# Kernel tuning notes

Hardware: AMD Instinct MI355X
Metric: run time of the kernel (lower is better)

## Reference

```python
import jax, jax.numpy as jnp
import numpy as np

WINDOW_SIZE = 11
SIGMA = 1.5
MAX_VAL = 1.0


def _gaussian_kernel2d(ws: int, sigma: float) -> jnp.ndarray:
    # matches kornia gaussian_t: x = arange(ws) - ws//2, normalized 1D, outer product
    x = jnp.arange(ws, dtype=jnp.float32) - ws // 2
    g = jnp.exp(-(x * x) / (2.0 * sigma * sigma))
    g = g / g.sum()
    return jnp.outer(g, g)  # (ws, ws)


def _filter2d(x: jnp.ndarray, kernel: jnp.ndarray) -> jnp.ndarray:
    # depthwise 'same' conv with reflect padding, matching kornia filter2d
    B, C, H, W = x.shape
    kh, kw = kernel.shape
    pad_h = ((kh - 1) // 2, (kh - 1) - (kh - 1) // 2)
    pad_w = ((kw - 1) // 2, (kw - 1) - (kw - 1) // 2)
    xp = jnp.pad(x, ((0, 0), (0, 0), pad_h, pad_w), mode='reflect')
    k = jnp.broadcast_to(kernel[None, None], (C, 1, kh, kw)).astype(x.dtype)
    return jax.lax.conv_general_dilated(
        xp, k, window_strides=(1, 1), padding='VALID',
        dimension_numbers=('NCHW', 'OIHW', 'NCHW'), feature_group_count=C)


def setup_inputs() -> dict:
    key = jax.random.key(0)
    k1, k2 = jax.random.split(key)
    img1 = jax.random.uniform(k1, (16, 3, 512, 512), dtype=jnp.float32)
    img2 = jax.random.uniform(k2, (16, 3, 512, 512), dtype=jnp.float32)
    kernel = _gaussian_kernel2d(WINDOW_SIZE, SIGMA)  # fixed gaussian window (11,11)
    return {"img1": img1, "img2": img2, "kernel": kernel}


def reference(img1, img2, kernel):
    C1 = (0.01 * MAX_VAL) ** 2
    C2 = (0.03 * MAX_VAL) ** 2
    mu1 = _filter2d(img1, kernel)
    mu2 = _filter2d(img2, kernel)
    mu1_sq = mu1 * mu1
    mu2_sq = mu2 * mu2
    mu1_mu2 = mu1 * mu2
    sigma1_sq = _filter2d(img1 * img1, kernel) - mu1_sq
    sigma2_sq = _filter2d(img2 * img2, kernel) - mu2_sq
    sigma12 = _filter2d(img1 * img2, kernel) - mu1_mu2
    num = (2.0 * mu1_mu2 + C1) * (2.0 * sigma12 + C2)
    den = (mu1_sq + mu2_sq + C1) * (sigma1_sq + sigma2_sq + C2)
    return num / den  # (B, C, H, W) SSIM map ('same' padding -> no crop)
```

## Files before the change

### kernel.cpp

```cpp
#include <hip/hip_runtime.h>

namespace {

constexpr int Hd = 512, Wd = 512;
constexpr int TH = 32;
constexpr int G  = 4;
constexpr int NG = TH / G;
constexpr int RAD = 5, WS = 11;
constexpr int NIN = G + WS - 1;
constexpr int HSTR = 524;
constexpr float C1c = 1e-4f;
constexpr float C2c = 9e-4f;

__device__ __forceinline__ float rcp_fast(float x) { return __builtin_amdgcn_rcpf(x); }

__global__ __launch_bounds__(512, 2) void ssim_map_kernel(
    const float* __restrict__ img1,
    const float* __restrict__ img2,
    const float* __restrict__ kern,
    float* __restrict__ out)
{
    __shared__ float hbuf[5 * G * HSTR];

    const int tid   = threadIdx.x;
    const int row0  = blockIdx.x * TH;
    const long pbase = (long)blockIdx.y * (long)(Hd * Wd);

    float g[WS];
    {
        float s = 0.f;
#pragma unroll
        for (int j = 0; j < WS; ++j) s += kern[RAD * WS + j];
        const float inv = 1.0f / s;
#pragma unroll
        for (int j = 0; j < WS; ++j) g[j] = kern[RAD * WS + j] * inv;
    }

    const int c  = tid;
    const int hr = tid >> 7;
    const int hu = tid & 127;

    for (int grp = 0; grp < NG; ++grp) {
        float acc[5][G];
#pragma unroll
        for (int q = 0; q < 5; ++q)
#pragma unroll
            for (int r = 0; r < G; ++r) acc[q][r] = 0.f;

        const int ibase = row0 + grp * G - RAD;
#pragma unroll
        for (int j = 0; j < NIN; ++j) {
            int gr = ibase + j;
            gr = (gr < 0) ? -gr : gr;
            gr = (gr >= Hd) ? (2 * Hd - 2 - gr) : gr;
            const long off = pbase + (long)gr * Wd + c;
            const float a = img1[off];
            const float b = img2[off];
            const float p11 = a * a, p22 = b * b, p12 = a * b;
#pragma unroll
            for (int r = 0; r < G; ++r) {
                const int k = j - r;
                if (k >= 0 && k < WS) {
                    const float w = g[k];
                    acc[0][r] = fmaf(w, a,   acc[0][r]);
                    acc[1][r] = fmaf(w, b,   acc[1][r]);
                    acc[2][r] = fmaf(w, p11, acc[2][r]);
                    acc[3][r] = fmaf(w, p22, acc[3][r]);
                    acc[4][r] = fmaf(w, p12, acc[4][r]);
                }
            }
        }

        __syncthreads();

#pragma unroll
        for (int q = 0; q < 5; ++q)
#pragma unroll
            for (int r = 0; r < G; ++r)
                hbuf[(q * G + r) * HSTR + RAD + c] = acc[q][r];

        if (c >= 1 && c <= RAD) {
#pragma unroll
            for (int q = 0; q < 5; ++q)
#pragma unroll
                for (int r = 0; r < G; ++r)
                    hbuf[(q * G + r) * HSTR + RAD - c] = acc[q][r];
        } else if (c >= Wd - 1 - RAD && c <= Wd - 2) {
#pragma unroll
            for (int q = 0; q < 5; ++q)
#pragma unroll
                for (int r = 0; r < G; ++r)
                    hbuf[(q * G + r) * HSTR + RAD + 1022 - c] = acc[q][r];
        }

        __syncthreads();

        float hq[5][4];
#pragma unroll
        for (int q = 0; q < 5; ++q) {
            const float* base = &hbuf[(q * G + hr) * HSTR + 4 * hu];
            const float4 v0 = *(const float4*)(base);
            const float4 v1 = *(const float4*)(base + 4);
            const float4 v2 = *(const float4*)(base + 8);
            const float2 v3 = *(const float2*)(base + 12);
            const float f[14] = { v0.x, v0.y, v0.z, v0.w,
                                  v1.x, v1.y, v1.z, v1.w,
                                  v2.x, v2.y, v2.z, v2.w,
                                  v3.x, v3.y };
            float h0 = 0.f, h1 = 0.f, h2 = 0.f, h3 = 0.f;
#pragma unroll
            for (int k = 0; k < WS; ++k) {
                const float w = g[k];
                h0 = fmaf(w, f[k],     h0);
                h1 = fmaf(w, f[k + 1], h1);
                h2 = fmaf(w, f[k + 2], h2);
                h3 = fmaf(w, f[k + 3], h3);
            }
            hq[q][0] = h0; hq[q][1] = h1; hq[q][2] = h2; hq[q][3] = h3;
        }

        float res[4];
#pragma unroll
        for (int j = 0; j < 4; ++j) {
            const float m1 = hq[0][j], m2 = hq[1][j];
            const float m1s = m1 * m1, m2s = m2 * m2, m12 = m1 * m2;
            const float sg1 = hq[2][j] - m1s;
            const float sg2 = hq[3][j] - m2s;
            const float sg12 = hq[4][j] - m12;
            const float num = (2.f * m12 + C1c) * (2.f * sg12 + C2c);
            const float den = (m1s + m2s + C1c) * (sg1 + sg2 + C2c);
            res[j] = num * rcp_fast(den);
        }
        float4* po = (float4*)&out[pbase + (long)(row0 + grp * G + hr) * Wd + 4 * hu];
        *po = make_float4(res[0], res[1], res[2], res[3]);
    }
}

}

extern "C" void kernel_launch(void* const* d_in, const int* in_sizes, int n_in,
                              void* d_out, int out_size, void* d_ws, size_t ws_size,
                              hipStream_t stream) {
    const float* img1 = (const float*)d_in[0];
    const float* img2 = (const float*)d_in[1];
    const float* kern = (const float*)d_in[2];
    float* outp = (float*)d_out;
    dim3 grid(Hd / TH, 48);
    ssim_map_kernel<<<grid, dim3(512), 0, stream>>>(img1, img2, kern, outp);
}
```

Measured before the change: 174.6 us.

## Tile SSIM kernel by column halves with packed f32x2 FMAs and split shared buffers

Splits each row band into two 256-column tiles, each run by a 256-thread block, so occupancy and block count rise. Each thread loads a halo column through reflect indexing instead of mirroring results into shared memory afterwards. The img1/img2 and squared channels are packed into float2 vectors so the compiler can emit packed FMA instructions. Shared memory is laid out as interleaved pairs to allow wider LDS reads. The cost is redundant vertical work on the 10 halo columns per tile and a second strided loop iteration for a few threads.

```diff
diff --git a/kernel.cpp b/kernel.cpp
--- a/kernel.cpp
+++ b/kernel.cpp
@@ -2,29 +2,38 @@
 
 namespace {
 
+typedef __attribute__((ext_vector_type(2))) float f32x2;
+typedef __attribute__((ext_vector_type(4))) float f32x4;
+
 constexpr int Hd = 512, Wd = 512;
+constexpr int TW = 256;
 constexpr int TH = 32;
 constexpr int G  = 4;
 constexpr int NG = TH / G;
 constexpr int RAD = 5, WS = 11;
 constexpr int NIN = G + WS - 1;
-constexpr int HSTR = 524;
+constexpr int SC  = TW + 2*RAD;
+constexpr int HSTR = 268;
 constexpr float C1c = 1e-4f;
 constexpr float C2c = 9e-4f;
 
 __device__ __forceinline__ float rcp_fast(float x) { return __builtin_amdgcn_rcpf(x); }
 
-__global__ __launch_bounds__(512, 2) void ssim_map_kernel(
+__global__ __launch_bounds__(256, 8) void ssim_map_kernel(
     const float* __restrict__ img1,
     const float* __restrict__ img2,
     const float* __restrict__ kern,
     float* __restrict__ out)
 {
-    __shared__ float hbuf[5 * G * HSTR];
+    __shared__ __align__(16) f32x2 hb01[G * HSTR];
+    __shared__ __align__(16) f32x2 hb23[G * HSTR];
+    __shared__ __align__(16) float hb4 [G * HSTR];
 
-    const int tid   = threadIdx.x;
-    const int row0  = blockIdx.x * TH;
-    const long pbase = (long)blockIdx.y * (long)(Hd * Wd);
+    const int tid  = threadIdx.x;
+    const int cb   = blockIdx.x;
+    const int row0 = blockIdx.y * TH;
+    const long pbase = (long)blockIdx.z * (long)(Hd * Wd);
+    const int col0 = cb * TW;
 
     float g[WS];
     {
@@ -36,103 +45,134 @@
         for (int j = 0; j < WS; ++j) g[j] = kern[RAD * WS + j] * inv;
     }
 
-    const int c  = tid;
-    const int hr = tid >> 7;
-    const int hu = tid & 127;
+    const int hr = tid >> 6;
+    const int hu = tid & 63;
 
     for (int grp = 0; grp < NG; ++grp) {
-        float acc[5][G];
-#pragma unroll
-        for (int q = 0; q < 5; ++q)
-#pragma unroll
-            for (int r = 0; r < G; ++r) acc[q][r] = 0.f;
+        __syncthreads();
 
         const int ibase = row0 + grp * G - RAD;
-#pragma unroll
-        for (int j = 0; j < NIN; ++j) {
-            int gr = ibase + j;
-            gr = (gr < 0) ? -gr : gr;
-            gr = (gr >= Hd) ? (2 * Hd - 2 - gr) : gr;
-            const long off = pbase + (long)gr * Wd + c;
-            const float a = img1[off];
-            const float b = img2[off];
-            const float p11 = a * a, p22 = b * b, p12 = a * b;
+        for (int s = tid; s < SC; s += 256) {
+            int gc = col0 - RAD + s;
+            gc = (gc < 0) ? -gc : gc;
+            gc = (gc >= Wd) ? (2 * Wd - 2 - gc) : gc;
+
+            f32x2 a01[G], a23[G]; float a4[G];
 #pragma unroll
             for (int r = 0; r < G; ++r) {
-                const int k = j - r;
-                if (k >= 0 && k < WS) {
-                    const float w = g[k];
-                    acc[0][r] = fmaf(w, a,   acc[0][r]);
-                    acc[1][r] = fmaf(w, b,   acc[1][r]);
-                    acc[2][r] = fmaf(w, p11, acc[2][r]);
-                    acc[3][r] = fmaf(w, p22, acc[3][r]);
-                    acc[4][r] = fmaf(w, p12, acc[4][r]);
+                a01[r].x = 0.f; a01[r].y = 0.f;
+                a23[r].x = 0.f; a23[r].y = 0.f;
+                a4[r] = 0.f;
+            }
+#pragma unroll
+            for (int j = 0; j < NIN; ++j) {
+                int gr = ibase + j;
+                gr = (gr < 0) ? -gr : gr;
+                gr = (gr >= Hd) ? (2 * Hd - 2 - gr) : gr;
+                const long off = pbase + (long)gr * Wd + gc;
+                const float a = img1[off];
+                const float b = img2[off];
+                f32x2 ab; ab.x = a; ab.y = b;
+                const f32x2 pp = ab * ab;
+                const float p12 = a * b;
+#pragma unroll
+                for (int r = 0; r < G; ++r) {
+                    const int k = j - r;
+                    if (k >= 0 && k < WS) {
+                        f32x2 w2; w2.x = g[k]; w2.y = g[k];
+                        a01[r] = __builtin_elementwise_fma(w2, ab, a01[r]);
+                        a23[r] = __builtin_elementwise_fma(w2, pp, a23[r]);
+                        a4[r]  = fmaf(g[k], p12, a4[r]);
+                    }
                 }
+            }
+#pragma unroll
+            for (int r = 0; r < G; ++r) {
+                hb01[r * HSTR + s] = a01[r];
+                hb23[r * HSTR + s] = a23[r];
+                hb4 [r * HSTR + s] = a4[r];
             }
         }
 
         __syncthreads();
 
+        f32x2 h01[4], h23[4];
+        float h4[4];
+        {
+            const f32x4* p4 = (const f32x4*)&hb01[hr * HSTR + 4 * hu];
+            f32x2 f[14];
 #pragma unroll
-        for (int q = 0; q < 5; ++q)
+            for (int i = 0; i < 7; ++i) {
+                const f32x4 t = p4[i];
+                f[2*i]   = t.lo;
+                f[2*i+1] = t.hi;
+            }
 #pragma unroll
-            for (int r = 0; r < G; ++r)
-                hbuf[(q * G + r) * HSTR + RAD + c] = acc[q][r];
-
-        if (c >= 1 && c <= RAD) {
+            for (int j = 0; j < 4; ++j) { h01[j].x = 0.f; h01[j].y = 0.f; }
 #pragma unroll
-            for (int q = 0; q < 5; ++q)
+            for (int k = 0; k < WS; ++k) {
+                f32x2 w2; w2.x = g[k]; w2.y = g[k];
 #pragma unroll
-                for (int r = 0; r < G; ++r)
-                    hbuf[(q * G + r) * HSTR + RAD - c] = acc[q][r];
-        } else if (c >= Wd - 1 - RAD && c <= Wd - 2) {
+                for (int j = 0; j < 4; ++j)
+                    h01[j] = __builtin_elementwise_fma(w2, f[k + j], h01[j]);
+            }
+        }
+        {
+            const f32x4* p4 = (const f32x4*)&hb23[hr * HSTR + 4 * hu];
+            f32x2 f[14];
 #pragma unroll
-            for (int q = 0; q < 5; ++q)
+            for (int i = 0; i < 7; ++i) {
+                const f32x4 t = p4[i];
+                f[2*i]   = t.lo;
+                f[2*i+1] = t.hi;
+            }
 #pragma unroll
-                for (int r = 0; r < G; ++r)
-                    hbuf[(q * G + r) * HSTR + RAD + 1022 - c] = acc[q][r];
+            for (int j = 0; j < 4; ++j) { h23[j].x = 0.f; h23[j].y = 0.f; }
+#pragma unroll
+            for (int k = 0; k < WS; ++k) {
+                f32x2 w2; w2.x = g[k]; w2.y = g[k];
+#pragma unroll
+                for (int j = 0; j < 4; ++j)
+                    h23[j] = __builtin_elementwise_fma(w2, f[k + j], h23[j]);
+            }
         }
-
-        __syncthreads();
-
-        float hq[5][4];
-#pragma unroll
-        for (int q = 0; q < 5; ++q) {
-            const float* base = &hbuf[(q * G + hr) * HSTR + 4 * hu];
-            const float4 v0 = *(const float4*)(base);
-            const float4 v1 = *(const float4*)(base + 4);
-            const float4 v2 = *(const float4*)(base + 8);
-            const float2 v3 = *(const float2*)(base + 12);
+        {
+            const float* base = &hb4[hr * HSTR + 4 * hu];
+            const f32x4 v0 = *(const f32x4*)(base);
+            const f32x4 v1 = *(const f32x4*)(base + 4);
+            const f32x4 v2 = *(const f32x4*)(base + 8);
+            const f32x2 v3 = *(const f32x2*)(base + 12);
             const float f[14] = { v0.x, v0.y, v0.z, v0.w,
                                   v1.x, v1.y, v1.z, v1.w,
                                   v2.x, v2.y, v2.z, v2.w,
                                   v3.x, v3.y };
-            float h0 = 0.f, h1 = 0.f, h2 = 0.f, h3 = 0.f;
+#pragma unroll
+            for (int j = 0; j < 4; ++j) h4[j] = 0.f;
 #pragma unroll
             for (int k = 0; k < WS; ++k) {
                 const float w = g[k];
-                h0 = fmaf(w, f[k],     h0);
-                h1 = fmaf(w, f[k + 1], h1);
-                h2 = fmaf(w, f[k + 2], h2);
-                h3 = fmaf(w, f[k + 3], h3);
+#pragma unroll
+                for (int j = 0; j < 4; ++j)
+                    h4[j] = fmaf(w, f[k + j], h4[j]);
             }
-            hq[q][0] = h0; hq[q][1] = h1; hq[q][2] = h2; hq[q][3] = h3;
         }
 
-        float res[4];
+        f32x4 res;
+        float rr[4];
 #pragma unroll
         for (int j = 0; j < 4; ++j) {
-            const float m1 = hq[0][j], m2 = hq[1][j];
-            const float m1s = m1 * m1, m2s = m2 * m2, m12 = m1 * m2;
-            const float sg1 = hq[2][j] - m1s;
-            const float sg2 = hq[3][j] - m2s;
-            const float sg12 = hq[4][j] - m12;
+            const f32x2 mm  = h01[j];
+            const f32x2 msq = mm * mm;
+            const f32x2 sg  = h23[j] - msq;
+            const float m12  = mm.x * mm.y;
+            const float sg12 = h4[j] - m12;
             const float num = (2.f * m12 + C1c) * (2.f * sg12 + C2c);
-            const float den = (m1s + m2s + C1c) * (sg1 + sg2 + C2c);
-            res[j] = num * rcp_fast(den);
+            const float den = (msq.x + msq.y + C1c) * (sg.x + sg.y + C2c);
+            rr[j] = num * rcp_fast(den);
         }
-        float4* po = (float4*)&out[pbase + (long)(row0 + grp * G + hr) * Wd + 4 * hu];
-        *po = make_float4(res[0], res[1], res[2], res[3]);
+        res.x = rr[0]; res.y = rr[1]; res.z = rr[2]; res.w = rr[3];
+        f32x4* po = (f32x4*)&out[pbase + (long)(row0 + grp * G + hr) * Wd + col0 + 4 * hu];
+        *po = res;
     }
 }
 
@@ -145,6 +185,6 @@
     const float* img2 = (const float*)d_in[1];
     const float* kern = (const float*)d_in[2];
     float* outp = (float*)d_out;
-    dim3 grid(Hd / TH, 48);
-    ssim_map_kernel<<<grid, dim3(512), 0, stream>>>(img1, img2, kern, outp);
+    dim3 grid(Wd / TW, Hd / TH, 48);
+    ssim_map_kernel<<<grid, dim3(256), 0, stream>>>(img1, img2, kern, outp);
 }
```

Measured after the change: 224.6 us. 28.6% more time.
